# Kernel tuning notes

Hardware: AMD Instinct MI355X
Metric: run time of the kernel (lower is better)

## Reference

```python
import jax, jax.numpy as jnp
import numpy as np

D_IN = 512
D_OUT = 512
NUM_HEADS = 8
HEAD_DIM = D_OUT // NUM_HEADS


def setup_inputs() -> dict:
    key = jax.random.key(0)
    ks = jax.random.split(key, 6)
    b, t, n = 4, 32, 256
    scale = 1.0 / np.sqrt(D_IN)
    return {
        "x": jax.random.normal(ks[0], (b, t, n, D_IN), dtype=jnp.float32),
        "Wq": jax.random.normal(ks[1], (D_IN, D_OUT), dtype=jnp.float32) * scale,
        "Wk": jax.random.normal(ks[2], (D_IN, D_OUT), dtype=jnp.float32) * scale,
        "Wv": jax.random.normal(ks[3], (D_IN, D_OUT), dtype=jnp.float32) * scale,
        "Wo": jax.random.normal(ks[4], (D_OUT, D_OUT), dtype=jnp.float32) * scale,
        "bo": jax.random.normal(ks[5], (D_OUT,), dtype=jnp.float32) * 0.01,
    }


def reference(x, Wq, Wk, Wv, Wo, bo):
    b, t, n, _ = x.shape
    h, hd = NUM_HEADS, HEAD_DIM
    # QKV projections (no bias, qkv_bias=False)
    q = (x @ Wq).reshape(b, t, n, h, hd)
    k = (x @ Wk).reshape(b, t, n, h, hd)
    v = (x @ Wv).reshape(b, t, n, h, hd)
    # attention over tokens, per (batch, timestamp, head)
    scores = jnp.einsum('btqhd,btkhd->bthqk', q, k) / np.sqrt(hd).astype(jnp.float32)
    weights = jax.nn.softmax(scores, axis=-1)
    # dropout p=0.0 (eval / deterministic reference) -> identity
    ctx = jnp.einsum('bthqk,btkhd->btqhd', weights, v).reshape(b, t, n, D_OUT)
    return ctx @ Wo + bo
```

## Files before the change

### kernel.cpp

```cpp
#include <hip/hip_runtime.h>
#include <hip/hip_bf16.h>

typedef __attribute__((ext_vector_type(8))) short bf16x8;
typedef __attribute__((ext_vector_type(4))) float f32x4;

#define MFMA_16x16x32(a,b,c) __builtin_amdgcn_mfma_f32_16x16x32_bf16((a),(b),(c),0,0,0)

__device__ __forceinline__ unsigned short f2bf(float f){
  unsigned int u = __float_as_uint(f);
  u += 0x7FFFu + ((u >> 16) & 1u);
  return (unsigned short)(u >> 16);
}

__device__ __forceinline__ unsigned int cvtpk_bf16(float lo, float hi){
  unsigned int r;
  asm("v_cvt_pk_bf16_f32 %0, %1, %2" : "=v"(r) : "v"(lo), "v"(hi));
  return r;
}

__device__ __forceinline__ void async16(const void* g, void* l){
  __builtin_amdgcn_global_load_lds((const __attribute__((address_space(1))) void*)g,
                                   (__attribute__((address_space(3))) void*)l,
                                   16, 0, 0);
}

#define FENCE asm volatile("" ::: "memory")
#define BARRL do{ asm volatile("s_waitcnt lgkmcnt(0)" ::: "memory"); \
                  __builtin_amdgcn_s_barrier(); FENCE; }while(0)

__global__ __launch_bounds__(256) void convert_all(const float* __restrict__ x,
                                                   const float* __restrict__ Wq,
                                                   const float* __restrict__ Wk,
                                                   const float* __restrict__ Wv,
                                                   const float* __restrict__ Wo,
                                                   unsigned short* __restrict__ xb,
                                                   unsigned short* __restrict__ WqkvT,
                                                   unsigned short* __restrict__ WoT){
  int idx = blockIdx.x*256 + threadIdx.x;
  int stride = gridDim.x*256;
  const int n4 = 16777216/4;
  for (int i = idx; i < n4; i += stride){
    float4 v = reinterpret_cast<const float4*>(x)[i];
    ushort4 o;
    o.x = f2bf(v.x); o.y = f2bf(v.y); o.z = f2bf(v.z); o.w = f2bf(v.w);
    reinterpret_cast<ushort4*>(xb)[i] = o;
  }
  const int T1 = 1536*512;
  const int total = T1 + 512*512;
  for (int o = idx; o < total; o += stride){
    if (o < T1){
      int n = o >> 9, k = o & 511;
      const float* W = (n < 512) ? Wq : ((n < 1024) ? Wk : Wv);
      WqkvT[o] = f2bf(W[k*512 + (n & 511)]);
    } else {
      int o2 = o - T1;
      int n = o2 >> 9, k = o2 & 511;
      WoT[o2] = f2bf(Wo[k*512 + n]);
    }
  }
}

template<int K, bool BIAS, bool OUTBF16>
__global__ __launch_bounds__(512, 2) void gemm4(const unsigned short* __restrict__ A,
                                                const unsigned short* __restrict__ Bt,
                                                float* __restrict__ Cf, unsigned short* __restrict__ Cb,
                                                const float* __restrict__ bias,
                                                int NB, int ldc){
  __shared__ __attribute__((aligned(16))) char ldsA[2][16384];
  __shared__ __attribute__((aligned(16))) char ldsB[2][16384];
  const int tid = threadIdx.x;
  const int lane = tid & 63, w = tid >> 6;
  const int wr = w >> 1, wc = w & 1;
  const int l15 = lane & 15, lhi = lane >> 4;

  const int cpx = gridDim.x >> 3;
  const int bid = (blockIdx.x & 7) * cpx + (blockIdx.x >> 3);
  const int bm = bid / NB, bn = bid % NB;

  const int row0 = tid >> 3;
  const int srcb = ((tid & 7) << 4) ^ ((row0 & 7) << 4);
  constexpr size_t rK2 = (size_t)K * 2;
  const char* Ab = (const char*)(A + (size_t)(bm*128 + row0) * K) + srcb;
  const char* Bb = (const char*)(Bt + (size_t)(bn*128 + row0) * K) + srcb;

#define STG_A(p,kt) do{ _Pragma("unroll") for (int j=0;j<2;++j) \
    async16(Ab + (size_t)(j*64)*rK2 + (size_t)(kt)*2, ldsA[p] + j*8192 + w*1024); }while(0)
#define STG_B(p,kt) do{ _Pragma("unroll") for (int j=0;j<2;++j) \
    async16(Bb + (size_t)(j*64)*rK2 + (size_t)(kt)*2, ldsB[p] + j*8192 + w*1024); }while(0)

#define LDAF(p) do{ _Pragma("unroll") for (int f=0;f<2;++f){ \
    const int m_ = wr*32 + f*16 + l15; \
    const char* base_ = ldsA[p] + m_*128; \
    af[f][0] = *reinterpret_cast<const bf16x8*>(base_ + (((lhi<<4))      ^ ((m_&7)<<4))); \
    af[f][1] = *reinterpret_cast<const bf16x8*>(base_ + ((64 + (lhi<<4)) ^ ((m_&7)<<4))); } }while(0)
#define LDBF(dst, p, nh) do{ _Pragma("unroll") for (int n2=0;n2<2;++n2){ \
    const int n_ = wc*64 + ((nh)*2+n2)*16 + l15; \
    const char* base_ = ldsB[p] + n_*128; \
    dst[n2][0] = *reinterpret_cast<const bf16x8*>(base_ + (((lhi<<4))      ^ ((n_&7)<<4))); \
    dst[n2][1] = *reinterpret_cast<const bf16x8*>(base_ + ((64 + (lhi<<4)) ^ ((n_&7)<<4))); } }while(0)
#define MFQ(nh, B_) do{ _Pragma("unroll") for (int f=0;f<2;++f) \
    _Pragma("unroll") for (int n2=0;n2<2;++n2) \
    _Pragma("unroll") for (int kk=0;kk<2;++kk) \
      acc[f][(nh)*2+n2] = MFMA_16x16x32(af[f][kk], B_[n2][kk], acc[f][(nh)*2+n2]); }while(0)

  f32x4 acc[2][4];
  const f32x4 fzero = {0.f,0.f,0.f,0.f};
  #pragma unroll
  for (int i=0;i<2;++i)
    #pragma unroll
    for (int j=0;j<4;++j) acc[i][j] = fzero;
  bf16x8 af[2][2], bf0[2][2], bfc[2][2];
  constexpr int nt = K >> 6;

  STG_A(0,0); STG_B(0,0); STG_A(1,64); STG_B(1,64);
  asm volatile("s_waitcnt vmcnt(4)" ::: "memory");
  __builtin_amdgcn_s_barrier(); FENCE;

  #pragma unroll
  for (int t = 0; t < nt; ++t){
    const int p = t & 1;
    const int kt2 = (t+2) << 6;
    LDAF(p); LDBF(bf0, p, 0); LDBF(bfc, p, 1);
    __builtin_amdgcn_s_setprio(1); MFQ(0, bf0); __builtin_amdgcn_s_setprio(0);
    BARRL;
    if (t+2 < nt){ STG_A(p, kt2); STG_B(p, kt2); }
    __builtin_amdgcn_s_setprio(1); MFQ(1, bfc); __builtin_amdgcn_s_setprio(0);
    if (t+1 < nt){
      if (t+2 < nt) asm volatile("s_waitcnt vmcnt(4) lgkmcnt(0)" ::: "memory");
      else          asm volatile("s_waitcnt vmcnt(0) lgkmcnt(0)" ::: "memory");
      __builtin_amdgcn_s_barrier(); FENCE;
    }
  }

  #pragma unroll
  for (int mi=0;mi<2;++mi){
    const int r = bm*128 + wr*32 + mi*16 + lhi*4;
    #pragma unroll
    for (int ni=0;ni<4;++ni){
      const int cc = bn*128 + wc*64 + ni*16 + l15;
      float bv = 0.f;
      if (BIAS) bv = bias[cc];
      #pragma unroll
      for (int i=0;i<4;++i){
        float v = acc[mi][ni][i] + bv;
        if (OUTBF16) Cb[(size_t)(r+i)*ldc + cc] = f2bf(v);
        else         Cf[(size_t)(r+i)*ldc + cc] = v;
      }
    }
  }
#undef STG_A
#undef STG_B
#undef LDAF
#undef LDBF
#undef MFQ
}

__global__ __launch_bounds__(256) void attn_kernel(const unsigned short* __restrict__ qkv,
                                                   unsigned short* __restrict__ ctx){
  __shared__ __attribute__((aligned(16))) unsigned short Ks[256*64];
  __shared__ __attribute__((aligned(16))) unsigned short Vst[64*264];

  const int bid = blockIdx.x;
  const int h = bid & 7, bt = bid >> 3;
  const int r0 = bt << 8;
  const int tid = threadIdx.x;
  const int lane = tid & 63, w = tid >> 6;
  const int l15 = lane & 15, lhi = lane >> 4;
  const char* qkvB = (const char*)qkv;
  const f32x4 fzero = {0.f,0.f,0.f,0.f};

  bf16x8 qf[4][2];
  #pragma unroll
  for (int st=0; st<4; ++st){
    int q0 = w*64 + st*16;
    #pragma unroll
    for (int kk=0; kk<2; ++kk)
      qf[st][kk] = *reinterpret_cast<const bf16x8*>(
          qkvB + ((size_t)(r0 + q0 + l15)*1536 + h*64 + kk*32 + lhi*8)*2);
  }

  #pragma unroll
  for (int j=0;j<8;++j){
    int c = (w*8+j)*64 + lane;
    int tok = c >> 3;
    int src = ((c & 7) << 4) ^ ((tok & 7) << 4);
    async16(qkvB + ((size_t)(r0 + tok)*1536 + 512 + h*64)*2 + src,
            (char*)Ks + ((w*8+j) << 10));
  }
  {
    const char* vbase = qkvB + ((size_t)(r0 + tid)*1536 + 1024 + h*64)*2;
    #pragma unroll
    for (int j=0;j<8;++j){
      bf16x8 vv = *reinterpret_cast<const bf16x8*>(vbase + (j<<4));
      #pragma unroll
      for (int e=0;e<8;++e)
        Vst[(j*8+e)*264 + tid] = (unsigned short)vv[e];
    }
  }
  __syncthreads();

  const int ga2 = (lhi & 1) << 1;
  const int lA = l15 + (ga2 << 4);
  const int lB = lA + 16;
  const bool odd = (lhi >> 1) != 0;

  #pragma unroll
  for (int st=0; st<4; ++st){
    const int q0 = w*64 + st*16;

    f32x4 S[16];
    #pragma unroll
    for (int t=0;t<16;++t) S[t] = fzero;
    #pragma unroll
    for (int kk=0;kk<2;++kk){
      #pragma unroll
      for (int t=0;t<16;++t){
        int tok = t*16 + l15;
        int off = tok*128 + (((kk<<6) + (lhi<<4)) ^ ((tok & 7) << 4));
        bf16x8 kf = *reinterpret_cast<const bf16x8*>((const char*)Ks + off);
        S[t] = MFMA_16x16x32(kf, qf[st][kk], S[t]);
      }
    }

    float m = S[0][0];
    #pragma unroll
    for (int t=0;t<16;++t)
      #pragma unroll
      for (int i=0;i<4;++i) m = fmaxf(m, S[t][i]);
    m = fmaxf(m, __shfl_xor(m, 16));
    m = fmaxf(m, __shfl_xor(m, 32));

    float l = 0.f;
    unsigned int P2[32];
    #pragma unroll
    for (int t=0;t<16;++t){
      float p0 = __expf((S[t][0] - m) * 0.125f);
      float p1 = __expf((S[t][1] - m) * 0.125f);
      float p2 = __expf((S[t][2] - m) * 0.125f);
      float p3 = __expf((S[t][3] - m) * 0.125f);
      l += (p0 + p1) + (p2 + p3);
      P2[2*t]   = cvtpk_bf16(p0, p1);
      P2[2*t+1] = cvtpk_bf16(p2, p3);
    }
    l += __shfl_xor(l, 16);
    l += __shfl_xor(l, 32);
    float rl = 1.0f / l;

    f32x4 O[4];
    #pragma unroll
    for (int dt=0;dt<4;++dt) O[dt] = fzero;
    #pragma unroll
    for (int s=0;s<8;++s){
      unsigned int a0e = __shfl((int)P2[4*s+0], lA), a0o = __shfl((int)P2[4*s+2], lA);
      unsigned int a1e = __shfl((int)P2[4*s+1], lA), a1o = __shfl((int)P2[4*s+3], lA);
      unsigned int b0e = __shfl((int)P2[4*s+0], lB), b0o = __shfl((int)P2[4*s+2], lB);
      unsigned int b1e = __shfl((int)P2[4*s+1], lB), b1o = __shfl((int)P2[4*s+3], lB);
      unsigned int u0 = odd ? a0o : a0e;
      unsigned int u1 = odd ? a1o : a1e;
      unsigned int u2 = odd ? b0o : b0e;
      unsigned int u3 = odd ? b1o : b1e;
      bf16x8 pa;
      reinterpret_cast<unsigned int*>(&pa)[0] = u0;
      reinterpret_cast<unsigned int*>(&pa)[1] = u1;
      reinterpret_cast<unsigned int*>(&pa)[2] = u2;
      reinterpret_cast<unsigned int*>(&pa)[3] = u3;
      #pragma unroll
      for (int dt=0;dt<4;++dt){
        bf16x8 vb = *reinterpret_cast<const bf16x8*>(&Vst[(dt*16 + l15)*264 + s*32 + 8*lhi]);
        O[dt] = MFMA_16x16x32(pa, vb, O[dt]);
      }
    }

    float rl4[4];
    #pragma unroll
    for (int i=0;i<4;++i) rl4[i] = __shfl(rl, lhi*4 + i);
    #pragma unroll
    for (int dt=0;dt<4;++dt){
      int col = h*64 + dt*16 + l15;
      #pragma unroll
      for (int i=0;i<4;++i){
        int row = r0 + q0 + lhi*4 + i;
        ctx[(size_t)row*512 + col] = f2bf(O[dt][i] * rl4[i]);
      }
    }
  }
}

extern "C" void kernel_launch(void* const* d_in, const int* in_sizes, int n_in,
                              void* d_out, int out_size, void* d_ws, size_t ws_size,
                              hipStream_t stream) {
  const float* x  = (const float*)d_in[0];
  const float* Wq = (const float*)d_in[1];
  const float* Wk = (const float*)d_in[2];
  const float* Wv = (const float*)d_in[3];
  const float* Wo = (const float*)d_in[4];
  const float* bo = (const float*)d_in[5];
  float* out = (float*)d_out;

  char* ws = (char*)d_ws;
  unsigned short* xb    = (unsigned short*)ws;
  unsigned short* qkv   = (unsigned short*)(ws + 33554432);
  unsigned short* WqkvT = (unsigned short*)(ws + 134217728);
  unsigned short* WoT   = (unsigned short*)(ws + 135790592);
  unsigned short* ctx   = xb;

  convert_all<<<2048, 256, 0, stream>>>(x, Wq, Wk, Wv, Wo, xb, WqkvT, WoT);
  gemm4<512, false, true><<<3072, 512, 0, stream>>>(xb, WqkvT, nullptr, qkv, nullptr, 12, 1536);
  attn_kernel<<<1024, 256, 0, stream>>>(qkv, ctx);
  gemm4<512, true, false><<<1024, 512, 0, stream>>>(ctx, WoT, out, nullptr, bo, 4, 512);
}
```

Before: 160.0 us.

## Double-buffer GEMM LDS fragments in registers to prefetch the next k-tile

Reworks the projection GEMM main loop so the A and B fragments for the next k-tile are read from LDS into a second register set while the second half of the current tile's MFMAs run. The loop is unrolled by two to alternate between the register sets, and the barriers and waitcnts are reordered to match. The aim is to hide LDS read latency behind matrix math. The cost is higher VGPR pressure and a more delicate barrier ordering between the global-to-LDS staging and the fragment reads.

```diff
diff --git a/kernel.cpp b/kernel.cpp
--- a/kernel.cpp
+++ b/kernel.cpp
@@ -88,20 +88,20 @@
 #define STG_B(p,kt) do{ _Pragma("unroll") for (int j=0;j<2;++j) \
     async16(Bb + (size_t)(j*64)*rK2 + (size_t)(kt)*2, ldsB[p] + j*8192 + w*1024); }while(0)
 
-#define LDAF(p) do{ _Pragma("unroll") for (int f=0;f<2;++f){ \
+#define LDAF_T(dst, p) do{ _Pragma("unroll") for (int f=0;f<2;++f){ \
     const int m_ = wr*32 + f*16 + l15; \
     const char* base_ = ldsA[p] + m_*128; \
-    af[f][0] = *reinterpret_cast<const bf16x8*>(base_ + (((lhi<<4))      ^ ((m_&7)<<4))); \
-    af[f][1] = *reinterpret_cast<const bf16x8*>(base_ + ((64 + (lhi<<4)) ^ ((m_&7)<<4))); } }while(0)
-#define LDBF(dst, p, nh) do{ _Pragma("unroll") for (int n2=0;n2<2;++n2){ \
+    dst[f][0] = *reinterpret_cast<const bf16x8*>(base_ + (((lhi<<4))      ^ ((m_&7)<<4))); \
+    dst[f][1] = *reinterpret_cast<const bf16x8*>(base_ + ((64 + (lhi<<4)) ^ ((m_&7)<<4))); } }while(0)
+#define LDBF_T(dst, p, nh) do{ _Pragma("unroll") for (int n2=0;n2<2;++n2){ \
     const int n_ = wc*64 + ((nh)*2+n2)*16 + l15; \
     const char* base_ = ldsB[p] + n_*128; \
     dst[n2][0] = *reinterpret_cast<const bf16x8*>(base_ + (((lhi<<4))      ^ ((n_&7)<<4))); \
     dst[n2][1] = *reinterpret_cast<const bf16x8*>(base_ + ((64 + (lhi<<4)) ^ ((n_&7)<<4))); } }while(0)
-#define MFQ(nh, B_) do{ _Pragma("unroll") for (int f=0;f<2;++f) \
+#define MFQ(AF_, nh, B_) do{ _Pragma("unroll") for (int f=0;f<2;++f) \
     _Pragma("unroll") for (int n2=0;n2<2;++n2) \
     _Pragma("unroll") for (int kk=0;kk<2;++kk) \
-      acc[f][(nh)*2+n2] = MFMA_16x16x32(af[f][kk], B_[n2][kk], acc[f][(nh)*2+n2]); }while(0)
+      acc[f][(nh)*2+n2] = MFMA_16x16x32(AF_[f][kk], B_[n2][kk], acc[f][(nh)*2+n2]); }while(0)
 
   f32x4 acc[2][4];
   const f32x4 fzero = {0.f,0.f,0.f,0.f};
@@ -109,27 +109,33 @@
   for (int i=0;i<2;++i)
     #pragma unroll
     for (int j=0;j<4;++j) acc[i][j] = fzero;
-  bf16x8 af[2][2], bf0[2][2], bfc[2][2];
+  bf16x8 afA[2][2], afB[2][2], bfcA[2][2], bfcB[2][2], bf0[2][2];
   constexpr int nt = K >> 6;
 
   STG_A(0,0); STG_B(0,0); STG_A(1,64); STG_B(1,64);
   asm volatile("s_waitcnt vmcnt(4)" ::: "memory");
   __builtin_amdgcn_s_barrier(); FENCE;
-
-  #pragma unroll
-  for (int t = 0; t < nt; ++t){
-    const int p = t & 1;
-    const int kt2 = (t+2) << 6;
-    LDAF(p); LDBF(bf0, p, 0); LDBF(bfc, p, 1);
-    __builtin_amdgcn_s_setprio(1); MFQ(0, bf0); __builtin_amdgcn_s_setprio(0);
-    BARRL;
-    if (t+2 < nt){ STG_A(p, kt2); STG_B(p, kt2); }
-    __builtin_amdgcn_s_setprio(1); MFQ(1, bfc); __builtin_amdgcn_s_setprio(0);
-    if (t+1 < nt){
-      if (t+2 < nt) asm volatile("s_waitcnt vmcnt(4) lgkmcnt(0)" ::: "memory");
-      else          asm volatile("s_waitcnt vmcnt(0) lgkmcnt(0)" ::: "memory");
-      __builtin_amdgcn_s_barrier(); FENCE;
-    }
+  LDAF_T(afA, 0); LDBF_T(bf0, 0, 0); LDBF_T(bfcA, 0, 1);
+  BARRL;
+
+#define BODY(t_, p_, AFc, BFCc, AFn, BFCn) do{ \
+    constexpr int o_ = (p_) ^ 1; \
+    if ((t_)+2 < nt){ STG_A(p_, ((t_)+2) << 6); STG_B(p_, ((t_)+2) << 6); } \
+    __builtin_amdgcn_s_setprio(1); MFQ(AFc, 0, bf0); __builtin_amdgcn_s_setprio(0); \
+    if ((t_)+1 < nt){ \
+      if ((t_)+2 < nt) asm volatile("s_waitcnt vmcnt(4)" ::: "memory"); \
+      else             asm volatile("s_waitcnt vmcnt(0)" ::: "memory"); \
+      __builtin_amdgcn_s_barrier(); FENCE; \
+      LDAF_T(AFn, o_); LDBF_T(bf0, o_, 0); LDBF_T(BFCn, o_, 1); \
+    } \
+    __builtin_amdgcn_s_setprio(1); MFQ(AFc, 1, BFCc); __builtin_amdgcn_s_setprio(0); \
+    if ((t_)+1 < nt) BARRL;  \
+  }while(0)
+
+  #pragma unroll
+  for (int tt = 0; tt < nt; tt += 2){
+    BODY(tt,   0, afA, bfcA, afB, bfcB);
+    BODY(tt+1, 1, afB, bfcB, afA, bfcA);
   }
 
   #pragma unroll
@@ -148,10 +154,11 @@
       }
     }
   }
+#undef BODY
 #undef STG_A
 #undef STG_B
-#undef LDAF
-#undef LDBF
+#undef LDAF_T
+#undef LDBF_T
 #undef MFQ
 }
 
```

Result: no change. 160.4 us (+0.3%).
